# Performance work log

Measured on AMD Instinct MI355X. Metric: run time of the kernel, lower is better.

Reference implementation:

```python
import jax, jax.numpy as jnp
import numpy as np

N = 50000      # nodes
E = 800000     # edges
NFEAT = 128
NHID = 128
EPS = 1e-5     # BatchNorm eps


def setup_inputs() -> dict:
    key = jax.random.key(0)
    ks = jax.random.split(key, 16)
    def lin(k, fan_in, shape):
        return jax.random.uniform(k, shape, jnp.float32, -1.0, 1.0) / np.sqrt(fan_in)
    return {
        "x": jax.random.normal(ks[0], (N, NFEAT), jnp.float32),
        "edge_index": jax.random.randint(ks[1], (2, E), 0, N, jnp.int32),
        "edge_weight": jax.random.uniform(ks[2], (E,), jnp.float32),
        # GCNConv 1 (nfeat -> nhid)
        "W1": lin(ks[3], NFEAT, (NFEAT, NHID)), "b1": jnp.zeros((NHID,), jnp.float32),
        # GCNConv 2 (nhid -> nhid)
        "W2": lin(ks[4], NHID, (NHID, NHID)), "b2": jnp.zeros((NHID,), jnp.float32),
        # BatchNorm affine params
        "g1": jnp.ones((NHID,), jnp.float32), "be1": jnp.zeros((NHID,), jnp.float32),
        "g2": jnp.ones((NHID,), jnp.float32), "be2": jnp.zeros((NHID,), jnp.float32),
        # MLP head: fc1 (nfeat + 2*nhid -> nhid), fc2 (nhid -> 1)
        "Wf1": lin(ks[5], NFEAT + 2 * NHID, (NFEAT + 2 * NHID, NHID)),
        "bf1": lin(ks[6], NFEAT + 2 * NHID, (NHID,)),
        "Wf2": lin(ks[7], NHID, (NHID, 1)),
        "bf2": lin(ks[8], NHID, (1,)),
    }


def _gcn_conv(x, src, dst, w, W, b):
    """PyG GCNConv with add_self_loops=True and symmetric gcn_norm."""
    h = x @ W                                   # [N, out] linear first
    deg = jnp.zeros((N,), h.dtype).at[dst].add(w) + 1.0  # +1 self-loop weight
    dinv = jax.lax.rsqrt(deg)                   # deg^{-1/2}
    norm = dinv[src] * w * dinv[dst]            # [E]
    out = jnp.zeros_like(h).at[dst].add(h[src] * norm[:, None])  # scatter-add
    out = out + h * (dinv * dinv)[:, None]      # self-loop term dinv_i^2 * h_i
    return out + b


def _bn(x, g, b):  # training-mode BatchNorm1d over node dim (biased var)
    m = x.mean(axis=0)
    v = x.var(axis=0)
    return g * (x - m) * jax.lax.rsqrt(v + EPS) + b


def reference(x, edge_index, edge_weight, W1, b1, W2, b2, g1, be1, g2, be2,
              Wf1, bf1, Wf2, bf2):
    src, dst = edge_index[0], edge_index[1]
    h1 = _bn(jax.nn.relu(_gcn_conv(x, src, dst, edge_weight, W1, b1)), g1, be1)
    h2 = _bn(jax.nn.relu(_gcn_conv(h1, src, dst, edge_weight, W2, b2)), g2, be2)
    cat = jnp.concatenate([x, h1, h2], axis=1)          # [N, nfeat+2*nhid]
    out = jax.nn.relu(cat @ Wf1 + bf1)
    out = jax.nn.relu(out @ Wf2 + bf2)
    return out.reshape(-1)                              # [N]
```

## Files before the change

kernel.cpp:

```cpp
#include <hip/hip_runtime.h>
#include <hip/hip_bf16.h>
#include <hip/hip_fp16.h>

#define NN 50000
#define EE 800000
#define NPAD 50048
constexpr float BN_EPS = 1e-5f;

typedef float  f32x4  __attribute__((ext_vector_type(4)));
typedef short  s16x8  __attribute__((ext_vector_type(8)));
typedef __bf16 bf16x8 __attribute__((ext_vector_type(8)));

struct __align__(8) Edge { int s; float w; };

__device__ inline void split2(float f, short& h, short& l) {
    unsigned u  = __builtin_bit_cast(unsigned, f);
    unsigned hr = (u + 0x7fffu + ((u >> 16) & 1u)) >> 16;
    h = (short)hr;
    float hf = __builtin_bit_cast(float, hr << 16);
    float r  = f - hf;
    unsigned u2 = __builtin_bit_cast(unsigned, r);
    unsigned lr = (u2 + 0x7fffu + ((u2 >> 16) & 1u)) >> 16;
    l = (short)lr;
}
__device__ inline f32x4 mfma_bf16(s16x8 a, s16x8 b, f32x4 c) {
    return __builtin_amdgcn_mfma_f32_16x16x32_bf16(
        __builtin_bit_cast(bf16x8, a), __builtin_bit_cast(bf16x8, b), c, 0, 0, 0);
}

__global__ __launch_bounds__(256) void k_zero_int(int* p, int n) {
    int i = blockIdx.x * 256 + threadIdx.x;
    if (i < n) p[i] = 0;
}

__global__ __launch_bounds__(256) void k_hist_rank(const int* __restrict__ dst,
                                                   int* __restrict__ cnt4,
                                                   int* __restrict__ rank) {
    int e = blockIdx.x * 256 + threadIdx.x;
    if (e < EE) {
        int s = e & 3;
        rank[e] = atomicAdd(&cnt4[s * NPAD + dst[e]], 1);
    }
}
__global__ __launch_bounds__(256) void k_scan1(const int* __restrict__ cnt4,
                                               int* __restrict__ excl,
                                               int* __restrict__ blksum) {
    __shared__ int sh[256];
    int tid = threadIdx.x;
    int i = blockIdx.x * 256 + tid;
    int v = 0;
    if (i < NN)
        v = cnt4[i] + cnt4[NPAD + i] + cnt4[2 * NPAD + i] + cnt4[3 * NPAD + i];
    sh[tid] = v;
    __syncthreads();
    #pragma unroll
    for (int off = 1; off < 256; off <<= 1) {
        int x = (tid >= off) ? sh[tid - off] : 0;
        __syncthreads();
        sh[tid] += x;
        __syncthreads();
    }
    if (i < NN) excl[i] = sh[tid] - v;
    if (tid == 255) blksum[blockIdx.x] = sh[255];
}
__global__ __launch_bounds__(256) void k_shardoff(int* __restrict__ cnt4) {
    int i = blockIdx.x * 256 + threadIdx.x;
    if (i >= NN) return;
    int c0 = cnt4[i], c1 = cnt4[NPAD + i], c2 = cnt4[2 * NPAD + i];
    cnt4[i] = 0;
    cnt4[NPAD + i] = c0;
    cnt4[2 * NPAD + i] = c0 + c1;
    cnt4[3 * NPAD + i] = c0 + c1 + c2;
}
__global__ __launch_bounds__(256) void k_scan2(int* blksum, int nblk) {
    __shared__ int sh[256];
    int tid = threadIdx.x;
    sh[tid] = (tid < nblk) ? blksum[tid] : 0;
    __syncthreads();
    #pragma unroll
    for (int off = 1; off < 256; off <<= 1) {
        int x = (tid >= off) ? sh[tid - off] : 0;
        __syncthreads();
        sh[tid] += x;
        __syncthreads();
    }
    if (tid < nblk) blksum[tid] = sh[tid];
}
__global__ __launch_bounds__(256) void k_scan3(const int* __restrict__ excl,
                                               const int* __restrict__ blksum,
                                               int* __restrict__ rowptr) {
    int i = blockIdx.x * 256 + threadIdx.x;
    if (i < NN)
        rowptr[i] = excl[i] + (blockIdx.x > 0 ? blksum[blockIdx.x - 1] : 0);
    if (i == 0) rowptr[NN] = EE;
}
__global__ __launch_bounds__(256) void k_place2(const int* __restrict__ src,
                                                const int* __restrict__ dst,
                                                const float* __restrict__ w,
                                                const int* __restrict__ rowptr,
                                                const int* __restrict__ shardoff,
                                                const int* __restrict__ rank,
                                                Edge* __restrict__ csr_e) {
    int e = blockIdx.x * 256 + threadIdx.x;
    if (e >= EE) return;
    int d = dst[e];
    int s = e & 3;
    int slot = rowptr[d] + shardoff[s * NPAD + d] + rank[e];
    Edge ed; ed.s = src[e]; ed.w = w[e];
    csr_e[slot] = ed;
}
__global__ __launch_bounds__(256) void k_deg_dinv(const int* __restrict__ rowptr,
                                                  const Edge* __restrict__ csr_e,
                                                  float* __restrict__ dinv) {
    int i = blockIdx.x * 256 + threadIdx.x;
    if (i >= NN) return;
    int e0 = rowptr[i], e1 = rowptr[i + 1];
    float s = 1.0f;
    for (int e = e0; e < e1; e++) s += csr_e[e].w;
    dinv[i] = rsqrtf(s);
}
__global__ __launch_bounds__(256) void k_edge_coef(Edge* __restrict__ csr_e,
                                                   const float* __restrict__ dinv) {
    int e = blockIdx.x * 256 + threadIdx.x;
    if (e < EE) {
        Edge ed = csr_e[e];
        ed.w *= dinv[ed.s];
        csr_e[e] = ed;
    }
}

__device__ inline void cvt_one(const float* W, short* Th, short* Tl, int idx, int K) {
    int k = idx >> 7, c = idx & 127;
    short h, l;
    split2(W[idx], h, l);
    Th[c * K + k] = h;
    Tl[c * K + k] = l;
}
__global__ __launch_bounds__(256) void k_cvt_all(const float* __restrict__ W1,
                                                 const float* __restrict__ W2,
                                                 const float* __restrict__ Wf1,
                                                 short* W1th, short* W1tl,
                                                 short* W2th, short* W2tl,
                                                 short* Wfth, short* Wftl) {
    int idx = blockIdx.x * 256 + threadIdx.x;
    if (idx < 16384)       cvt_one(W1,  W1th, W1tl, idx, 128);
    else if (idx < 32768)  cvt_one(W2,  W2th, W2tl, idx - 16384, 128);
    else if (idx < 81920)  cvt_one(Wf1, Wfth, Wftl, idx - 32768, 384);
}

__global__ __launch_bounds__(256) void gemm_mfma(const float* __restrict__ X,
                                                 const float* __restrict__ sc,
                                                 const float* __restrict__ sh,
                                                 const short* __restrict__ WTh,
                                                 const short* __restrict__ WTl,
                                                 __half* __restrict__ Y, int n) {
    __shared__ __align__(16) short As[2][64][40];
    __shared__ __align__(16) short Bs[2][128][40];
    int tid  = threadIdx.x;
    int row0 = blockIdx.x * 64;
    int w = tid >> 6, lane = tid & 63;
    int wr = w >> 1, wc = w & 1;
    int fr = lane & 15, fq = lane >> 4;
    f32x4 acc[2][4] = {};
    for (int k0 = 0; k0 < 128; k0 += 32) {
        {
            int r = tid >> 2, seg = tid & 3;
            int gr = row0 + r;
            float f[8];
            if (gr < n) {
                float4 v0 = *(const float4*)&X[(size_t)gr * 128 + k0 + seg * 8];
                float4 v1 = *(const float4*)&X[(size_t)gr * 128 + k0 + seg * 8 + 4];
                f[0]=v0.x; f[1]=v0.y; f[2]=v0.z; f[3]=v0.w;
                f[4]=v1.x; f[5]=v1.y; f[6]=v1.z; f[7]=v1.w;
            } else {
                #pragma unroll
                for (int i = 0; i < 8; i++) f[i] = 0.f;
            }
            if (sc) {
                float scv[8], shv[8];
                *(float4*)&scv[0] = *(const float4*)&sc[k0 + seg * 8];
                *(float4*)&scv[4] = *(const float4*)&sc[k0 + seg * 8 + 4];
                *(float4*)&shv[0] = *(const float4*)&sh[k0 + seg * 8];
                *(float4*)&shv[4] = *(const float4*)&sh[k0 + seg * 8 + 4];
                #pragma unroll
                for (int i = 0; i < 8; i++) f[i] = fmaf(f[i], scv[i], shv[i]);
            }
            short h[8], l[8];
            #pragma unroll
            for (int i = 0; i < 8; i++) split2(f[i], h[i], l[i]);
            *(s16x8*)&As[0][r][seg * 8] = *(s16x8*)h;
            *(s16x8*)&As[1][r][seg * 8] = *(s16x8*)l;
        }
        #pragma unroll
        for (int rd = 0; rd < 2; rd++) {
            int idx = rd * 256 + tid;
            int c = idx >> 2, seg = idx & 3;
            *(s16x8*)&Bs[0][c][seg * 8] = *(const s16x8*)&WTh[c * 128 + k0 + seg * 8];
            *(s16x8*)&Bs[1][c][seg * 8] = *(const s16x8*)&WTl[c * 128 + k0 + seg * 8];
        }
        __syncthreads();
        s16x8 ah[2], al[2], bh[4], bl[4];
        #pragma unroll
        for (int m = 0; m < 2; m++) {
            int r = wr * 32 + m * 16 + fr;
            ah[m] = *(s16x8*)&As[0][r][fq * 8];
            al[m] = *(s16x8*)&As[1][r][fq * 8];
        }
        #pragma unroll
        for (int nf = 0; nf < 4; nf++) {
            int c = wc * 64 + nf * 16 + fr;
            bh[nf] = *(s16x8*)&Bs[0][c][fq * 8];
            bl[nf] = *(s16x8*)&Bs[1][c][fq * 8];
        }
        #pragma unroll
        for (int m = 0; m < 2; m++)
            #pragma unroll
            for (int nf = 0; nf < 4; nf++) {
                acc[m][nf] = mfma_bf16(ah[m], bh[nf], acc[m][nf]);
                acc[m][nf] = mfma_bf16(ah[m], bl[nf], acc[m][nf]);
                acc[m][nf] = mfma_bf16(al[m], bh[nf], acc[m][nf]);
            }
        __syncthreads();
    }
    #pragma unroll
    for (int m = 0; m < 2; m++)
        #pragma unroll
        for (int nf = 0; nf < 4; nf++)
            #pragma unroll
            for (int j = 0; j < 4; j++) {
                int gr = row0 + wr * 32 + m * 16 + fq * 4 + j;
                int gc = wc * 64 + nf * 16 + fr;
                if (gr < n) Y[(size_t)gr * 128 + gc] = __float2half(acc[m][nf][j]);
            }
}

__global__ __launch_bounds__(256) void gemm_head_mfma(const float* __restrict__ X0,
                                                      const float* __restrict__ X1,
                                                      const float* __restrict__ X2,
                                                      const float* __restrict__ sc1,
                                                      const float* __restrict__ sh1,
                                                      const float* __restrict__ sc2,
                                                      const float* __restrict__ sh2,
                                                      const short* __restrict__ WTh,
                                                      const short* __restrict__ WTl,
                                                      const float* __restrict__ bf1,
                                                      const float* __restrict__ Wf2,
                                                      const float* __restrict__ bf2,
                                                      float* __restrict__ out) {
    __shared__ __align__(16) short As[2][64][40];
    __shared__ __align__(16) short Bs[2][128][40];
    __shared__ float red[64];
    int tid  = threadIdx.x;
    int row0 = blockIdx.x * 64;
    int w = tid >> 6, lane = tid & 63;
    int wr = w >> 1, wc = w & 1;
    int fr = lane & 15, fq = lane >> 4;
    f32x4 acc[2][4] = {};
    for (int k0 = 0; k0 < 384; k0 += 32) {
        const float* S   = (k0 < 128) ? X0 : (k0 < 256) ? X1 : X2;
        const float* scp = (k0 < 128) ? nullptr : (k0 < 256) ? sc1 : sc2;
        const float* shp = (k0 < 128) ? nullptr : (k0 < 256) ? sh1 : sh2;
        int kb = k0 & 127;
        {
            int r = tid >> 2, seg = tid & 3;
            int gr = row0 + r;
            float f[8];
            if (gr < NN) {
                float4 v0 = *(const float4*)&S[(size_t)gr * 128 + kb + seg * 8];
                float4 v1 = *(const float4*)&S[(size_t)gr * 128 + kb + seg * 8 + 4];
                f[0]=v0.x; f[1]=v0.y; f[2]=v0.z; f[3]=v0.w;
                f[4]=v1.x; f[5]=v1.y; f[6]=v1.z; f[7]=v1.w;
            } else {
                #pragma unroll
                for (int i = 0; i < 8; i++) f[i] = 0.f;
            }
            if (scp) {
                float scv[8], shv[8];
                *(float4*)&scv[0] = *(const float4*)&scp[kb + seg * 8];
                *(float4*)&scv[4] = *(const float4*)&scp[kb + seg * 8 + 4];
                *(float4*)&shv[0] = *(const float4*)&shp[kb + seg * 8];
                *(float4*)&shv[4] = *(const float4*)&shp[kb + seg * 8 + 4];
                #pragma unroll
                for (int i = 0; i < 8; i++) f[i] = fmaf(f[i], scv[i], shv[i]);
            }
            short h[8], l[8];
            #pragma unroll
            for (int i = 0; i < 8; i++) split2(f[i], h[i], l[i]);
            *(s16x8*)&As[0][r][seg * 8] = *(s16x8*)h;
            *(s16x8*)&As[1][r][seg * 8] = *(s16x8*)l;
        }
        #pragma unroll
        for (int rd = 0; rd < 2; rd++) {
            int idx = rd * 256 + tid;
            int c = idx >> 2, seg = idx & 3;
            *(s16x8*)&Bs[0][c][seg * 8] = *(const s16x8*)&WTh[c * 384 + k0 + seg * 8];
            *(s16x8*)&Bs[1][c][seg * 8] = *(const s16x8*)&WTl[c * 384 + k0 + seg * 8];
        }
        __syncthreads();
        s16x8 ah[2], al[2], bh[4], bl[4];
        #pragma unroll
        for (int m = 0; m < 2; m++) {
            int r = wr * 32 + m * 16 + fr;
            ah[m] = *(s16x8*)&As[0][r][fq * 8];
            al[m] = *(s16x8*)&As[1][r][fq * 8];
        }
        #pragma unroll
        for (int nf = 0; nf < 4; nf++) {
            int c = wc * 64 + nf * 16 + fr;
            bh[nf] = *(s16x8*)&Bs[0][c][fq * 8];
            bl[nf] = *(s16x8*)&Bs[1][c][fq * 8];
        }
        #pragma unroll
        for (int m = 0; m < 2; m++)
            #pragma unroll
            for (int nf = 0; nf < 4; nf++) {
                acc[m][nf] = mfma_bf16(ah[m], bh[nf], acc[m][nf]);
                acc[m][nf] = mfma_bf16(ah[m], bl[nf], acc[m][nf]);
                acc[m][nf] = mfma_bf16(al[m], bh[nf], acc[m][nf]);
            }
        __syncthreads();
    }
    if (tid < 64) red[tid] = 0.f;
    __syncthreads();
    float ps[2][4] = {};
    #pragma unroll
    for (int m = 0; m < 2; m++)
        #pragma unroll
        for (int nf = 0; nf < 4; nf++) {
            int gc = wc * 64 + nf * 16 + fr;
            float b1v = bf1[gc];
            float w2v = Wf2[gc];
            #pragma unroll
            for (int j = 0; j < 4; j++) {
                float u = fmaxf(acc[m][nf][j] + b1v, 0.f);
                ps[m][j] = fmaf(u, w2v, ps[m][j]);
            }
        }
    #pragma unroll
    for (int off = 1; off <= 8; off <<= 1)
        #pragma unroll
        for (int m = 0; m < 2; m++)
            #pragma unroll
            for (int j = 0; j < 4; j++)
                ps[m][j] += __shfl_xor(ps[m][j], off, 64);
    if (fr == 0) {
        #pragma unroll
        for (int m = 0; m < 2; m++)
            #pragma unroll
            for (int j = 0; j < 4; j++)
                atomicAdd(&red[wr * 32 + m * 16 + fq * 4 + j], ps[m][j]);
    }
    __syncthreads();
    if (tid < 64 && row0 + tid < NN)
        out[row0 + tid] = fmaxf(red[tid] + bf2[0], 0.f);
}

__global__ __launch_bounds__(256) void k_agg_stats(const __half* __restrict__ t,
                                                   const float* __restrict__ dinv,
                                                   const float* __restrict__ b,
                                                   const int* __restrict__ rowptr,
                                                   const Edge* __restrict__ csr_e,
                                                   float* __restrict__ h,
                                                   float* __restrict__ partS,
                                                   float* __restrict__ partSS) {
    int wv   = threadIdx.x >> 6;
    int lane = threadIdx.x & 63;
    int sub  = lane >> 4;
    int sl   = lane & 15;
    float bb[8];
    *(float4*)&bb[0] = *(const float4*)&b[sl * 8];
    *(float4*)&bb[4] = *(const float4*)&b[sl * 8 + 4];
    float sS[8] = {}, sSS[8] = {};
    #pragma unroll 1
    for (int ni = 0; ni < 8; ni++) {
        int wid = blockIdx.x * 32 + wv * 8 + ni;
        if (wid >= NN) break;
        float di = dinv[wid];
        float acc[8];
        if (sub == 0) {
            s16x8 raw = *(const s16x8*)&t[(size_t)wid * 128 + sl * 8];
            union { s16x8 r; __half2 h2[4]; } u; u.r = raw;
            #pragma unroll
            for (int i = 0; i < 4; i++) {
                float2 f = __half22float2(u.h2[i]);
                acc[2 * i]     = f.x * di;
                acc[2 * i + 1] = f.y * di;
            }
        } else {
            #pragma unroll
            for (int i = 0; i < 8; i++) acc[i] = 0.f;
        }
        int e0 = rowptr[wid], e1 = rowptr[wid + 1];
        #pragma unroll 2
        for (int e = e0; e < e1; e += 4) {
            int ee   = e + sub;
            bool v   = ee < e1;
            Edge ed  = csr_e[v ? ee : e0];
            float cw = v ? ed.w : 0.f;
            s16x8 raw = *(const s16x8*)&t[(size_t)ed.s * 128 + sl * 8];
            union { s16x8 r; __half2 h2[4]; } u; u.r = raw;
            #pragma unroll
            for (int i = 0; i < 4; i++) {
                float2 f = __half22float2(u.h2[i]);
                acc[2 * i]     = fmaf(f.x, cw, acc[2 * i]);
                acc[2 * i + 1] = fmaf(f.y, cw, acc[2 * i + 1]);
            }
        }
        #pragma unroll
        for (int i = 0; i < 8; i++) {
            acc[i] += __shfl_xor(acc[i], 16, 64);
            acc[i] += __shfl_xor(acc[i], 32, 64);
        }
        if (sub == 0) {
            float hv[8];
            #pragma unroll
            for (int i = 0; i < 8; i++) {
                hv[i] = fmaxf(fmaf(acc[i], di, bb[i]), 0.f);
                sS[i]  += hv[i];
                sSS[i] += hv[i] * hv[i];
            }
            *(float4*)&h[(size_t)wid * 128 + sl * 8]     = *(float4*)&hv[0];
            *(float4*)&h[(size_t)wid * 128 + sl * 8 + 4] = *(float4*)&hv[4];
        }
    }
    __shared__ float s_s[4][128], s_ss[4][128];
    if (sub == 0) {
        #pragma unroll
        for (int i = 0; i < 8; i++) {
            s_s [wv][sl * 8 + i] = sS[i];
            s_ss[wv][sl * 8 + i] = sSS[i];
        }
    }
    __syncthreads();
    if (threadIdx.x < 128) {
        int c = threadIdx.x;
        float S  = s_s [0][c] + s_s [1][c] + s_s [2][c] + s_s [3][c];
        float SS = s_ss[0][c] + s_ss[1][c] + s_ss[2][c] + s_ss[3][c];
        partS [blockIdx.x * 128 + c] = S;
        partSS[blockIdx.x * 128 + c] = SS;
    }
}

__global__ __launch_bounds__(256) void k_stats(const float* __restrict__ partS,
                                               const float* __restrict__ partSS,
                                               int nblk,
                                               const float* __restrict__ g,
                                               const float* __restrict__ be,
                                               float* __restrict__ scale,
                                               float* __restrict__ shift) {
    int c   = blockIdx.x;
    int tid = threadIdx.x;
    float s = 0.f, ss = 0.f;
    for (int b = tid; b < nblk; b += 256) {
        s  += partS [b * 128 + c];
        ss += partSS[b * 128 + c];
    }
    #pragma unroll
    for (int off = 32; off > 0; off >>= 1) {
        s  += __shfl_down(s,  off, 64);
        ss += __shfl_down(ss, off, 64);
    }
    __shared__ float sh_s[4], sh_ss[4];
    int wv = tid >> 6, lane = tid & 63;
    if (lane == 0) { sh_s[wv] = s; sh_ss[wv] = ss; }
    __syncthreads();
    if (tid == 0) {
        float S  = sh_s[0]  + sh_s[1]  + sh_s[2]  + sh_s[3];
        float SS = sh_ss[0] + sh_ss[1] + sh_ss[2] + sh_ss[3];
        float mean = S / (float)NN;
        float var  = SS / (float)NN - mean * mean;
        float sc   = g[c] * rsqrtf(var + BN_EPS);
        scale[c] = sc;
        shift[c] = be[c] - mean * sc;
    }
}

extern "C" void kernel_launch(void* const* d_in, const int* in_sizes, int n_in,
                              void* d_out, int out_size, void* d_ws, size_t ws_size,
                              hipStream_t stream) {
    const float* x   = (const float*)d_in[0];
    const int*   ei  = (const int*)d_in[1];
    const float* ew  = (const float*)d_in[2];
    const float* W1  = (const float*)d_in[3];
    const float* b1  = (const float*)d_in[4];
    const float* W2  = (const float*)d_in[5];
    const float* b2  = (const float*)d_in[6];
    const float* g1  = (const float*)d_in[7];
    const float* be1 = (const float*)d_in[8];
    const float* g2  = (const float*)d_in[9];
    const float* be2 = (const float*)d_in[10];
    const float* Wf1 = (const float*)d_in[11];
    const float* bf1 = (const float*)d_in[12];
    const float* Wf2 = (const float*)d_in[13];
    const float* bf2 = (const float*)d_in[14];
    float* out = (float*)d_out;

    const int* src = ei;
    const int* dst = ei + EE;

    const int NAGG = (NN + 31) / 32;

    float* w = (float*)d_ws;
    __half* t      = (__half*)w;  w += (size_t)NN * 64;
    float* h1      = w;  w += (size_t)NN * 128;
    float* h2      = w;  w += (size_t)NN * 128;
    float* dinv    = w;  w += NPAD;
    float* partS   = w;  w += (size_t)NAGG * 128;
    float* partSS  = w;  w += (size_t)NAGG * 128;
    float* scale1  = w;  w += 128;
    float* shift1  = w;  w += 128;
    float* scale2  = w;  w += 128;
    float* shift2  = w;  w += 128;
    Edge* csr_e    = (Edge*)w;  w += 2 * (size_t)EE;
    int* iw        = (int*)w;
    int* rowptr    = iw; iw += 50056;
    int* cnt4      = iw; iw += 4 * NPAD;
    int* excl      = iw; iw += NPAD;
    int* blksum    = iw; iw += 256;
    short* sw      = (short*)iw;
    short* W1th = sw; sw += 128 * 128;
    short* W1tl = sw; sw += 128 * 128;
    short* W2th = sw; sw += 128 * 128;
    short* W2tl = sw; sw += 128 * 128;
    short* Wfth = sw; sw += 128 * 384;
    short* Wftl = sw; sw += 128 * 384;
    int* rank = (int*)t;

    const int GN = (NN + 255) / 256;
    const int GE = (EE + 255) / 256;
    const int NBLK = (NN + 63) / 64;

    k_cvt_all<<<(81920 + 255) / 256, 256, 0, stream>>>(W1, W2, Wf1, W1th, W1tl,
                                                       W2th, W2tl, Wfth, Wftl);
    k_zero_int<<<(4 * NPAD + 255) / 256, 256, 0, stream>>>(cnt4, 4 * NPAD);
    k_hist_rank<<<GE, 256, 0, stream>>>(dst, cnt4, rank);
    k_scan1<<<GN, 256, 0, stream>>>(cnt4, excl, blksum);
    k_shardoff<<<GN, 256, 0, stream>>>(cnt4);
    k_scan2<<<1, 256, 0, stream>>>(blksum, GN);
    k_scan3<<<GN, 256, 0, stream>>>(excl, blksum, rowptr);
    k_place2<<<GE, 256, 0, stream>>>(src, dst, ew, rowptr, cnt4, rank, csr_e);
    k_deg_dinv<<<GN, 256, 0, stream>>>(rowptr, csr_e, dinv);
    k_edge_coef<<<GE, 256, 0, stream>>>(csr_e, dinv);

    gemm_mfma<<<NBLK, 256, 0, stream>>>(x, nullptr, nullptr, W1th, W1tl, t, NN);
    k_agg_stats<<<NAGG, 256, 0, stream>>>(t, dinv, b1, rowptr, csr_e, h1, partS, partSS);
    k_stats<<<128, 256, 0, stream>>>(partS, partSS, NAGG, g1, be1, scale1, shift1);

    gemm_mfma<<<NBLK, 256, 0, stream>>>(h1, scale1, shift1, W2th, W2tl, t, NN);
    k_agg_stats<<<NAGG, 256, 0, stream>>>(t, dinv, b2, rowptr, csr_e, h2, partS, partSS);
    k_stats<<<128, 256, 0, stream>>>(partS, partSS, NAGG, g2, be2, scale2, shift2);

    gemm_head_mfma<<<NBLK, 256, 0, stream>>>(x, h1, h2, scale1, shift1, scale2, shift2,
                                             Wfth, Wftl, bf1, Wf2, bf2, out);
}
```

Measured before the change: 223.8 us.

## Merge init kernels, fold shard offsets into scan, and restructure BN stat reduction

Weight conversion and the zeroing of the histogram counters now run in a single launch, and the per-shard offset computation moves into the first scan kernel, which drops two launches. The BatchNorm stats reduction changes from 128 blocks doing strided column reads to a two-stage reduction. In the first stage 64 blocks each sum rows with coalesced reads across the channels, then one block finishes the reduction and computes scale and shift. The new scheme makes reads coalesced but adds a launch per BN layer and a small single-block tail.

```diff
diff --git a/kernel.cpp b/kernel.cpp
--- a/kernel.cpp
+++ b/kernel.cpp
@@ -28,9 +28,25 @@
         __builtin_bit_cast(bf16x8, a), __builtin_bit_cast(bf16x8, b), c, 0, 0, 0);
 }
 
-__global__ __launch_bounds__(256) void k_zero_int(int* p, int n) {
-    int i = blockIdx.x * 256 + threadIdx.x;
-    if (i < n) p[i] = 0;
+__device__ inline void cvt_one(const float* W, short* Th, short* Tl, int idx, int K) {
+    int k = idx >> 7, c = idx & 127;
+    short h, l;
+    split2(W[idx], h, l);
+    Th[c * K + k] = h;
+    Tl[c * K + k] = l;
+}
+__global__ __launch_bounds__(256) void k_init(const float* __restrict__ W1,
+                                              const float* __restrict__ W2,
+                                              const float* __restrict__ Wf1,
+                                              short* W1th, short* W1tl,
+                                              short* W2th, short* W2tl,
+                                              short* Wfth, short* Wftl,
+                                              int* __restrict__ cnt4) {
+    int idx = blockIdx.x * 256 + threadIdx.x;
+    if (idx < 16384)       cvt_one(W1,  W1th, W1tl, idx, 128);
+    else if (idx < 32768)  cvt_one(W2,  W2th, W2tl, idx - 16384, 128);
+    else if (idx < 81920)  cvt_one(Wf1, Wfth, Wftl, idx - 32768, 384);
+    if (idx < 4 * NPAD) cnt4[idx] = 0;
 }
 
 __global__ __launch_bounds__(256) void k_hist_rank(const int* __restrict__ dst,
@@ -42,15 +58,17 @@
         rank[e] = atomicAdd(&cnt4[s * NPAD + dst[e]], 1);
     }
 }
-__global__ __launch_bounds__(256) void k_scan1(const int* __restrict__ cnt4,
-                                               int* __restrict__ excl,
-                                               int* __restrict__ blksum) {
+__global__ __launch_bounds__(256) void k_scan1s(int* __restrict__ cnt4,
+                                                int* __restrict__ excl,
+                                                int* __restrict__ blksum) {
     __shared__ int sh[256];
     int tid = threadIdx.x;
     int i = blockIdx.x * 256 + tid;
-    int v = 0;
-    if (i < NN)
-        v = cnt4[i] + cnt4[NPAD + i] + cnt4[2 * NPAD + i] + cnt4[3 * NPAD + i];
+    int c0 = 0, c1 = 0, c2 = 0, c3 = 0;
+    if (i < NN) {
+        c0 = cnt4[i]; c1 = cnt4[NPAD + i]; c2 = cnt4[2 * NPAD + i]; c3 = cnt4[3 * NPAD + i];
+    }
+    int v = c0 + c1 + c2 + c3;
     sh[tid] = v;
     __syncthreads();
     #pragma unroll
@@ -60,17 +78,14 @@
         sh[tid] += x;
         __syncthreads();
     }
-    if (i < NN) excl[i] = sh[tid] - v;
+    if (i < NN) {
+        excl[i] = sh[tid] - v;
+        cnt4[i] = 0;
+        cnt4[NPAD + i] = c0;
+        cnt4[2 * NPAD + i] = c0 + c1;
+        cnt4[3 * NPAD + i] = c0 + c1 + c2;
+    }
     if (tid == 255) blksum[blockIdx.x] = sh[255];
-}
-__global__ __launch_bounds__(256) void k_shardoff(int* __restrict__ cnt4) {
-    int i = blockIdx.x * 256 + threadIdx.x;
-    if (i >= NN) return;
-    int c0 = cnt4[i], c1 = cnt4[NPAD + i], c2 = cnt4[2 * NPAD + i];
-    cnt4[i] = 0;
-    cnt4[NPAD + i] = c0;
-    cnt4[2 * NPAD + i] = c0 + c1;
-    cnt4[3 * NPAD + i] = c0 + c1 + c2;
 }
 __global__ __launch_bounds__(256) void k_scan2(int* blksum, int nblk) {
     __shared__ int sh[256];
@@ -127,25 +142,6 @@
         ed.w *= dinv[ed.s];
         csr_e[e] = ed;
     }
-}
-
-__device__ inline void cvt_one(const float* W, short* Th, short* Tl, int idx, int K) {
-    int k = idx >> 7, c = idx & 127;
-    short h, l;
-    split2(W[idx], h, l);
-    Th[c * K + k] = h;
-    Tl[c * K + k] = l;
-}
-__global__ __launch_bounds__(256) void k_cvt_all(const float* __restrict__ W1,
-                                                 const float* __restrict__ W2,
-                                                 const float* __restrict__ Wf1,
-                                                 short* W1th, short* W1tl,
-                                                 short* W2th, short* W2tl,
-                                                 short* Wfth, short* Wftl) {
-    int idx = blockIdx.x * 256 + threadIdx.x;
-    if (idx < 16384)       cvt_one(W1,  W1th, W1tl, idx, 128);
-    else if (idx < 32768)  cvt_one(W2,  W2th, W2tl, idx - 16384, 128);
-    else if (idx < 81920)  cvt_one(Wf1, Wfth, Wftl, idx - 32768, 384);
 }
 
 __global__ __launch_bounds__(256) void gemm_mfma(const float* __restrict__ X,
@@ -441,34 +437,39 @@
     }
 }
 
-__global__ __launch_bounds__(256) void k_stats(const float* __restrict__ partS,
-                                               const float* __restrict__ partSS,
-                                               int nblk,
-                                               const float* __restrict__ g,
-                                               const float* __restrict__ be,
-                                               float* __restrict__ scale,
-                                               float* __restrict__ shift) {
-    int c   = blockIdx.x;
-    int tid = threadIdx.x;
-    float s = 0.f, ss = 0.f;
-    for (int b = tid; b < nblk; b += 256) {
-        s  += partS [b * 128 + c];
-        ss += partSS[b * 128 + c];
-    }
+__global__ __launch_bounds__(256) void k_stats_p(const float* __restrict__ partS,
+                                                 const float* __restrict__ partSS,
+                                                 int nblk,
+                                                 float* __restrict__ pS,
+                                                 float* __restrict__ pSS) {
+    int c   = threadIdx.x & 127;
+    int sel = threadIdx.x >> 7;
+    const float* src = sel ? partSS : partS;
+    float a = 0.f;
+    for (int r = blockIdx.x; r < nblk; r += 64)
+        a += src[(size_t)r * 128 + c];
+    (sel ? pSS : pS)[blockIdx.x * 128 + c] = a;
+}
+
+__global__ __launch_bounds__(256) void k_stats_f(const float* __restrict__ pS,
+                                                 const float* __restrict__ pSS,
+                                                 const float* __restrict__ g,
+                                                 const float* __restrict__ be,
+                                                 float* __restrict__ scale,
+                                                 float* __restrict__ shift) {
+    __shared__ float tot[2][128];
+    int c   = threadIdx.x & 127;
+    int sel = threadIdx.x >> 7;
+    const float* src = sel ? pSS : pS;
+    float a = 0.f;
     #pragma unroll
-    for (int off = 32; off > 0; off >>= 1) {
-        s  += __shfl_down(s,  off, 64);
-        ss += __shfl_down(ss, off, 64);
-    }
-    __shared__ float sh_s[4], sh_ss[4];
-    int wv = tid >> 6, lane = tid & 63;
-    if (lane == 0) { sh_s[wv] = s; sh_ss[wv] = ss; }
+    for (int r = 0; r < 64; r++)
+        a += src[r * 128 + c];
+    tot[sel][c] = a;
     __syncthreads();
-    if (tid == 0) {
-        float S  = sh_s[0]  + sh_s[1]  + sh_s[2]  + sh_s[3];
-        float SS = sh_ss[0] + sh_ss[1] + sh_ss[2] + sh_ss[3];
-        float mean = S / (float)NN;
-        float var  = SS / (float)NN - mean * mean;
+    if (threadIdx.x < 128) {
+        float mean = tot[0][c] / (float)NN;
+        float var  = tot[1][c] / (float)NN - mean * mean;
         float sc   = g[c] * rsqrtf(var + BN_EPS);
         scale[c] = sc;
         shift[c] = be[c] - mean * sc;
@@ -507,6 +508,8 @@
     float* dinv    = w;  w += NPAD;
     float* partS   = w;  w += (size_t)NAGG * 128;
     float* partSS  = w;  w += (size_t)NAGG * 128;
+    float* pS      = w;  w += 64 * 128;
+    float* pSS     = w;  w += 64 * 128;
     float* scale1  = w;  w += 128;
     float* shift1  = w;  w += 128;
     float* scale2  = w;  w += 128;
@@ -530,12 +533,10 @@
     const int GE = (EE + 255) / 256;
     const int NBLK = (NN + 63) / 64;
 
-    k_cvt_all<<<(81920 + 255) / 256, 256, 0, stream>>>(W1, W2, Wf1, W1th, W1tl,
-                                                       W2th, W2tl, Wfth, Wftl);
-    k_zero_int<<<(4 * NPAD + 255) / 256, 256, 0, stream>>>(cnt4, 4 * NPAD);
+    k_init<<<(4 * NPAD + 255) / 256, 256, 0, stream>>>(W1, W2, Wf1, W1th, W1tl,
+                                                       W2th, W2tl, Wfth, Wftl, cnt4);
     k_hist_rank<<<GE, 256, 0, stream>>>(dst, cnt4, rank);
-    k_scan1<<<GN, 256, 0, stream>>>(cnt4, excl, blksum);
-    k_shardoff<<<GN, 256, 0, stream>>>(cnt4);
+    k_scan1s<<<GN, 256, 0, stream>>>(cnt4, excl, blksum);
     k_scan2<<<1, 256, 0, stream>>>(blksum, GN);
     k_scan3<<<GN, 256, 0, stream>>>(excl, blksum, rowptr);
     k_place2<<<GE, 256, 0, stream>>>(src, dst, ew, rowptr, cnt4, rank, csr_e);
@@ -544,11 +545,13 @@
 
     gemm_mfma<<<NBLK, 256, 0, stream>>>(x, nullptr, nullptr, W1th, W1tl, t, NN);
     k_agg_stats<<<NAGG, 256, 0, stream>>>(t, dinv, b1, rowptr, csr_e, h1, partS, partSS);
-    k_stats<<<128, 256, 0, stream>>>(partS, partSS, NAGG, g1, be1, scale1, shift1);
+    k_stats_p<<<64, 256, 0, stream>>>(partS, partSS, NAGG, pS, pSS);
+    k_stats_f<<<1, 256, 0, stream>>>(pS, pSS, g1, be1, scale1, shift1);
 
     gemm_mfma<<<NBLK, 256, 0, stream>>>(h1, scale1, shift1, W2th, W2tl, t, NN);
     k_agg_stats<<<NAGG, 256, 0, stream>>>(t, dinv, b2, rowptr, csr_e, h2, partS, partSS);
-    k_stats<<<128, 256, 0, stream>>>(partS, partSS, NAGG, g2, be2, scale2, shift2);
+    k_stats_p<<<64, 256, 0, stream>>>(partS, partSS, NAGG, pS, pSS);
+    k_stats_f<<<1, 256, 0, stream>>>(pS, pSS, g2, be2, scale2, shift2);
 
     gemm_head_mfma<<<NBLK, 256, 0, stream>>>(x, h1, h2, scale1, shift1, scale2, shift2,
                                              Wfth, Wftl, bf1, Wf2, bf2, out);
```

Result: slower. 230.6 us (+3.0%).
